# Kernel tuning notes

Measured on AMD Instinct MI355X. Metric: run time of the kernel, lower is better.

Reference implementation:

```python
import jax, jax.numpy as jnp
import numpy as np

B, S, D = 4, 2048, 512
H, HD, RL = 8, 64, 64   # nheads, head_dim = D//H, rl_dim
TEMPER = 1.0
BETA = 1.0
SLOPE = 0.01  # LeakyReLU negative slope
LN_EPS = 1e-5


def setup_inputs() -> dict:
    key = jax.random.key(0)
    ks = jax.random.split(key, 12)
    scale = 0.02
    return {
        "h":   jax.random.normal(ks[0], (B, S, D), dtype=jnp.float32),
        "rh":  jax.random.normal(ks[1], (B, S, RL), dtype=jnp.float32),
        "Wl":  jax.random.normal(ks[2], (D, D), dtype=jnp.float32) * scale,   # linear_l (in,out)
        "Wr":  jax.random.normal(ks[3], (D, D), dtype=jnp.float32) * scale,   # linear_r
        "al":  jax.random.normal(ks[4], (HD,), dtype=jnp.float32) * scale,    # att_l: Linear(head_dim,1)
        "ar":  jax.random.normal(ks[5], (HD,), dtype=jnp.float32) * scale,    # att_r
        "Wrs": jax.random.normal(ks[6], (RL, RL * H), dtype=jnp.float32) * scale,  # r_source
        "Wrt": jax.random.normal(ks[7], (RL, RL * H), dtype=jnp.float32) * scale,  # r_target
        "Wf":  jax.random.normal(ks[8], (D, D), dtype=jnp.float32) * scale,   # linear_final
        "ln_g": jnp.ones((D,), dtype=jnp.float32),
        "ln_b": jnp.zeros((D,), dtype=jnp.float32),
    }


def _layer_norm(x, g, b):
    mu = jnp.mean(x, axis=-1, keepdims=True)
    var = jnp.mean(jnp.square(x - mu), axis=-1, keepdims=True)
    return (x - mu) * jax.lax.rsqrt(var + LN_EPS) * g + b


def reference(h, rh, Wl, Wr, al, ar, Wrs, Wrt, Wf, ln_g, ln_b):
    leaky = lambda x: jnp.where(x >= 0, x, SLOPE * x)
    # projections -> [B, H, S, HD]
    fl = (h @ Wl).reshape(B, S, H, HD).transpose(0, 2, 1, 3)
    fr = (h @ Wr).reshape(B, S, H, HD).transpose(0, 2, 1, 3)
    # additive attention logits: [B,H,S,1] + [B,H,1,S]
    sl = jnp.einsum('bhsd,d->bhs', leaky(fl), al)
    sr = jnp.einsum('bhsd,d->bhs', leaky(fr), ar)
    score = sl[:, :, :, None] + sr[:, :, None, :]
    # relation-embedding bilinear bias: r_k @ r_q -> [B,H,S,S]
    r_k = (rh @ Wrs).reshape(B, S, H, RL).transpose(0, 2, 1, 3)   # [B,H,S,RL]
    r_q = (rh @ Wrt).reshape(B, S, H, RL).transpose(0, 2, 3, 1)   # [B,H,RL,S]
    score = score + BETA * jnp.einsum('bhsr,bhrt->bhst', r_k, r_q)
    score = jax.nn.softmax(score / TEMPER, axis=-1)
    # context and output projection (dropout = 0 -> identity)
    context = jnp.einsum('bhst,bhtd->bhsd', score, fr)
    h_sa = context.transpose(0, 2, 1, 3).reshape(B, S, H * HD)
    fh = h_sa @ Wf
    return _layer_norm(h + fh, ln_g, ln_b)
```

## Files before the change

kernel.cpp:

```cpp
#include <hip/hip_runtime.h>
#include <math.h>

#define B_ 4
#define S_ 2048
#define D_ 512
#define H_ 8
#define HD_ 64
#define RL_ 64
#define LN_EPS 1e-5f
#define SLOPE 0.01f
#define LOG2E 1.4426950408889634f

typedef __attribute__((ext_vector_type(8))) __bf16 bf16x8;
typedef __attribute__((ext_vector_type(4))) float f32x4;

__device__ __forceinline__ float leaky(float x) { return x >= 0.f ? x : SLOPE * x; }

__device__ __forceinline__ ushort f2bf(float f) {
    union { float f; unsigned u; } v; v.f = f;
    unsigned r = v.u + 0x7fffu + ((v.u >> 16) & 1u);
    return (ushort)(r >> 16);
}

__device__ __forceinline__ void g2lds16(const void* g, void* l) {
    __builtin_amdgcn_global_load_lds(
        (const __attribute__((address_space(1))) void*)(uintptr_t)g,
        (__attribute__((address_space(3))) void*)(uintptr_t)l, 16, 0, 0);
}

__global__ __launch_bounds__(256) void prep(
    const float* __restrict__ h, const float* __restrict__ rh,
    const float* __restrict__ Wr, const float* __restrict__ Wf,
    const float* __restrict__ Wrs, const float* __restrict__ Wrt,
    ushort* __restrict__ hb, ushort* __restrict__ rhb,
    ushort* __restrict__ WrT, ushort* __restrict__ WfT,
    ushort* __restrict__ WrsT, ushort* __restrict__ WrtT)
{
    const int bx = blockIdx.x, tid = threadIdx.x;
    if (bx < 4608) {
        const float* in = (bx < 4096) ? h : rh;
        ushort* o = (bx < 4096) ? hb : rhb;
        const int i = (bx < 4096 ? bx : bx - 4096) * 256 + tid;
        const float4 v = ((const float4*)in)[i];
        ushort4 u; u.x = f2bf(v.x); u.y = f2bf(v.y); u.z = f2bf(v.z); u.w = f2bf(v.w);
        ((ushort4*)o)[i] = u;
    } else if (bx < 6656) {
        const float* in = (bx < 5632) ? Wr : Wf;
        ushort* o = (bx < 5632) ? WrT : WfT;
        const int idx = (bx - (bx < 5632 ? 4608 : 5632)) * 256 + tid;
        const int k = idx & 511, n = idx >> 9;
        o[idx] = f2bf(in[k * 512 + n]);
    } else {
        const float* in = (bx < 6784) ? Wrs : Wrt;
        ushort* o = (bx < 6784) ? WrsT : WrtT;
        const int idx = (bx - (bx < 6784 ? 6656 : 6784)) * 256 + tid;
        const int k = idx & 63, n = idx >> 6;
        o[idx] = f2bf(in[k * 512 + n]);
    }
}

template <int MODE>
__global__ __launch_bounds__(256) void mfma_gemm(
    const ushort* __restrict__ A, const ushort* __restrict__ WT,
    void* __restrict__ Cout, float* __restrict__ sred,
    const float* __restrict__ avec, int K, float scale,
    const ushort* __restrict__ WT2, void* __restrict__ Cout2, float scale2)
{
    __shared__ ushort As[64 * 32];
    __shared__ ushort Bs[128 * 32];

    const int tid = threadIdx.x;
    const int lane = tid & 63, w = tid >> 6;
    const int ln = lane & 15, quad = lane >> 4;
    const int wm = w >> 1, wn = w & 1;
    const int m0 = blockIdx.x * 64, n0 = blockIdx.y * 128;

    const ushort* wt = WT; void* co = Cout; float scl = scale;
    if constexpr (MODE == 3) {
        if (blockIdx.z) { wt = WT2; co = Cout2; scl = scale2; }
    }

    const int srA = tid >> 2;
    const int lchA = ((lane & 3) - (srA >> 1)) & 3;
    const ushort* Ag = A + (size_t)(m0 + srA) * K + lchA * 8;
    ushort* AsL = As + (size_t)tid * 8;
    const int srB = w * 32 + (lane >> 2);
    const int lchB = ((lane & 3) - (srB >> 1)) & 3;
    const ushort* Bg0 = wt + (size_t)(n0 + srB) * K + lchB * 8;
    const ushort* Bg1 = Bg0 + (size_t)16 * K;
    ushort* BsL = Bs + srB * 32 + (lane & 3) * 8;

    const int pc = (quad + (ln >> 1)) & 3;

    f32x4 acc[2][4] = {};
    for (int k0 = 0; k0 < K; k0 += 32) {
        __syncthreads();
        g2lds16(Ag, AsL);
        g2lds16(Bg0, BsL); g2lds16(Bg1, BsL + 512);
        Ag += 32; Bg0 += 32; Bg1 += 32;
        __syncthreads();

        bf16x8 af[2], bfr[4];
        #pragma unroll
        for (int mi = 0; mi < 2; ++mi)
            af[mi] = *(const bf16x8*)&As[(wm * 32 + mi * 16 + ln) * 32 + pc * 8];
        #pragma unroll
        for (int ni = 0; ni < 4; ++ni)
            bfr[ni] = *(const bf16x8*)&Bs[(wn * 64 + ni * 16 + ln) * 32 + pc * 8];
        #pragma unroll
        for (int mi = 0; mi < 2; ++mi)
            #pragma unroll
            for (int ni = 0; ni < 4; ++ni)
                acc[mi][ni] = __builtin_amdgcn_mfma_f32_16x16x32_bf16(
                    af[mi], bfr[ni], acc[mi][ni], 0, 0, 0);
    }

    if constexpr (MODE == 0) {
        float* C = (float*)co;
        #pragma unroll
        for (int mi = 0; mi < 2; ++mi) {
            const int row = m0 + wm * 32 + mi * 16 + quad * 4;
            #pragma unroll
            for (int ni = 0; ni < 4; ++ni) {
                const int col = n0 + wn * 64 + ni * 16 + ln;
                #pragma unroll
                for (int r = 0; r < 4; ++r)
                    C[(size_t)(row + r) * 512 + col] = acc[mi][ni][r];
            }
        }
    }
    if constexpr (MODE == 2 || MODE == 3) {
        const int head = blockIdx.y * 2 + wn;
        const int b = m0 >> 11;
        const size_t bh = (size_t)b * H_ + head;
        if constexpr (MODE == 2) {
            ushort* frT = (ushort*)co;
            #pragma unroll
            for (int mi = 0; mi < 2; ++mi) {
                const int s = (m0 & (S_ - 1)) + wm * 32 + mi * 16 + quad * 4;
                #pragma unroll
                for (int ni = 0; ni < 4; ++ni) {
                    const int d = ni * 16 + ln;
                    ushort4 o;
                    o.x = f2bf(acc[mi][ni][0]); o.y = f2bf(acc[mi][ni][1]);
                    o.z = f2bf(acc[mi][ni][2]); o.w = f2bf(acc[mi][ni][3]);
                    *(ushort4*)(frT + (bh * 64 + d) * S_ + s) = o;
                }
            }
            float a4[4];
            #pragma unroll
            for (int ni = 0; ni < 4; ++ni) a4[ni] = avec[ni * 16 + ln];
            #pragma unroll
            for (int mi = 0; mi < 2; ++mi) {
                const int s = (m0 & (S_ - 1)) + wm * 32 + mi * 16 + quad * 4;
                #pragma unroll
                for (int r = 0; r < 4; ++r) {
                    float v = 0.f;
                    #pragma unroll
                    for (int ni = 0; ni < 4; ++ni)
                        v += leaky(acc[mi][ni][r]) * a4[ni];
                    #pragma unroll
                    for (int off = 8; off; off >>= 1) v += __shfl_xor(v, off, 16);
                    if (ln == 0) sred[bh * S_ + s + r] = v * scl;
                }
            }
        }
        if constexpr (MODE == 3) {
            ushort* O = (ushort*)co;
            #pragma unroll
            for (int mi = 0; mi < 2; ++mi) {
                const int s = (m0 & (S_ - 1)) + wm * 32 + mi * 16 + quad * 4;
                #pragma unroll
                for (int ni = 0; ni < 4; ++ni) {
                    const int d = ni * 16 + ln;
                    #pragma unroll
                    for (int r = 0; r < 4; ++r)
                        O[(bh * S_ + s + r) * 64 + d] = f2bf(acc[mi][ni][r] * scl);
                }
            }
        }
    }
}

__global__ __launch_bounds__(256) void attn_mfma(
    const ushort* __restrict__ frT, const ushort* __restrict__ rk,
    const ushort* __restrict__ rq, const float* __restrict__ sr,
    ushort* __restrict__ hsa)
{
    __shared__ ushort RQ[2][64][64];
    __shared__ ushort FT[2][64][64];
    __shared__ ushort PS[8][16][72];
    __shared__ float SRs[S_];

    const int tid = threadIdx.x;
    const int w = tid >> 6;
    const int lane = tid & 63;
    const int ln = lane & 15;
    const int quad = lane >> 4;
    const int b = blockIdx.z, h = blockIdx.y, q0 = blockIdx.x * 128;
    const size_t bh = (size_t)b * H_ + h;

    for (int i = tid; i < S_; i += 256) SRs[i] = sr[bh * S_ + i];

    const ushort* rkb = rk + ((bh * S_ + q0 + w * 32) << 6);
    bf16x8 a[2][2];
    #pragma unroll
    for (int qs = 0; qs < 2; ++qs) {
        const ushort* p = rkb + (qs * 16 + ln) * 64 + quad * 8;
        a[qs][0] = *(const bf16x8*)p;
        a[qs][1] = *(const bf16x8*)(p + 32);
    }

    const ushort* rqb = rq + (bh * S_ << 6);
    const ushort* ftb = frT + (size_t)bh * 64 * S_;

    const int rl = lane >> 3;
    const int sg = ((lane & 7) - rl) & 7;
    const int row0 = w * 16 + rl;

    #define STAGE(buf, t0)                                                        \
        {                                                                         \
            _Pragma("unroll")                                                     \
            for (int i = 0; i < 2; ++i) {                                         \
                const int tr = row0 + i * 8;                                      \
                g2lds16(rqb + ((size_t)((t0) + tr) << 6) + sg * 8,                \
                        &RQ[buf][tr][(lane & 7) * 8]);                            \
                g2lds16(ftb + (size_t)tr * S_ + (t0) + sg * 8,                    \
                        &FT[buf][tr][(lane & 7) * 8]);                            \
            }                                                                     \
        }

    STAGE(0, 0)
    __syncthreads();

    float lsum[2][4] = {};
    f32x4 ctx[2][4] = {};
    int buf = 0;

    for (int t0 = 0; t0 < S_; t0 += 64) {
        if (t0 + 64 < S_) STAGE(buf ^ 1, t0 + 64)

        f32x4 sc[2][4];
        #pragma unroll
        for (int jb = 0; jb < 4; ++jb) {
            const int tr = 16 * jb + ln;
            const bf16x8 b0 = *(const bf16x8*)&RQ[buf][tr][((quad + tr) & 7) * 8];
            const bf16x8 b1 = *(const bf16x8*)&RQ[buf][tr][((quad + 4 + tr) & 7) * 8];
            #pragma unroll
            for (int qs = 0; qs < 2; ++qs) {
                f32x4 t = {0.f, 0.f, 0.f, 0.f};
                t = __builtin_amdgcn_mfma_f32_16x16x32_bf16(a[qs][0], b0, t, 0, 0, 0);
                t = __builtin_amdgcn_mfma_f32_16x16x32_bf16(a[qs][1], b1, t, 0, 0, 0);
                sc[qs][jb] = t;
            }
        }

        float srv[4];
        #pragma unroll
        for (int jb = 0; jb < 4; ++jb) srv[jb] = SRs[t0 + 16 * jb + ln];

        #pragma unroll
        for (int qs = 0; qs < 2; ++qs)
            #pragma unroll
            for (int r = 0; r < 4; ++r) {
                const int prow = quad * 4 + r;
                float psum = 0.f;
                #pragma unroll
                for (int jb = 0; jb < 4; ++jb) {
                    const float p = __builtin_amdgcn_exp2f(sc[qs][jb][r] + srv[jb]);
                    psum += p;
                    union { float f; unsigned u; } v; v.f = p;
                    PS[w * 2 + qs][prow][16 * jb + ln] = (ushort)(v.u >> 16);
                }
                lsum[qs][r] += psum;
            }

        bf16x8 fb0[4], fb1[4];
        #pragma unroll
        for (int jb = 0; jb < 4; ++jb) {
            const int dr = 16 * jb + ln;
            fb0[jb] = *(const bf16x8*)&FT[buf][dr][((quad + dr) & 7) * 8];
            fb1[jb] = *(const bf16x8*)&FT[buf][dr][((quad + 4 + dr) & 7) * 8];
        }
        #pragma unroll
        for (int qs = 0; qs < 2; ++qs) {
            const bf16x8 pa0 = *(const bf16x8*)&PS[w * 2 + qs][ln][quad * 8];
            const bf16x8 pa1 = *(const bf16x8*)&PS[w * 2 + qs][ln][32 + quad * 8];
            #pragma unroll
            for (int jb = 0; jb < 4; ++jb) {
                ctx[qs][jb] = __builtin_amdgcn_mfma_f32_16x16x32_bf16(pa0, fb0[jb], ctx[qs][jb], 0, 0, 0);
                ctx[qs][jb] = __builtin_amdgcn_mfma_f32_16x16x32_bf16(pa1, fb1[jb], ctx[qs][jb], 0, 0, 0);
            }
        }

        __syncthreads();
        buf ^= 1;
    }

    #pragma unroll
    for (int qs = 0; qs < 2; ++qs)
        #pragma unroll
        for (int r = 0; r < 4; ++r) {
            float l = lsum[qs][r];
            #pragma unroll
            for (int off = 8; off; off >>= 1) l += __shfl_xor(l, off, 16);
            const float inv = 1.f / l;
            const int q = q0 + w * 32 + qs * 16 + quad * 4 + r;
            ushort* orow = hsa + (size_t)(b * S_ + q) * D_ + h * 64;
            #pragma unroll
            for (int jb = 0; jb < 4; ++jb)
                orow[16 * jb + ln] = f2bf(ctx[qs][jb][r] * inv);
        }
}

__global__ __launch_bounds__(256) void ln_kernel(
    const float* __restrict__ h, const float* __restrict__ fh,
    const float* __restrict__ g, const float* __restrict__ bb,
    float* __restrict__ out)
{
    const int row = blockIdx.x, tid = threadIdx.x;
    const float* hp = h + (size_t)row * 512;
    const float* fp = fh + (size_t)row * 512;
    const float x0 = hp[tid] + fp[tid];
    const float x1 = hp[tid + 256] + fp[tid + 256];
    __shared__ float red[4];

    float s = x0 + x1;
    #pragma unroll
    for (int off = 32; off; off >>= 1) s += __shfl_xor(s, off, 64);
    if ((tid & 63) == 0) red[tid >> 6] = s;
    __syncthreads();
    const float mu = (red[0] + red[1] + red[2] + red[3]) * (1.f / 512.f);

    const float d0 = x0 - mu, d1 = x1 - mu;
    float v = d0 * d0 + d1 * d1;
    #pragma unroll
    for (int off = 32; off; off >>= 1) v += __shfl_xor(v, off, 64);
    __syncthreads();
    if ((tid & 63) == 0) red[tid >> 6] = v;
    __syncthreads();
    const float var = (red[0] + red[1] + red[2] + red[3]) * (1.f / 512.f);
    const float inv = rsqrtf(var + LN_EPS);

    out[(size_t)row * 512 + tid] = d0 * inv * g[tid] + bb[tid];
    out[(size_t)row * 512 + tid + 256] = d1 * inv * g[tid + 256] + bb[tid + 256];
}

extern "C" void kernel_launch(void* const* d_in, const int* in_sizes, int n_in,
                              void* d_out, int out_size, void* d_ws, size_t ws_size,
                              hipStream_t stream)
{
    const float* h   = (const float*)d_in[0];
    const float* rh  = (const float*)d_in[1];
    const float* Wr  = (const float*)d_in[3];
    const float* ar  = (const float*)d_in[5];
    const float* Wrs = (const float*)d_in[6];
    const float* Wrt = (const float*)d_in[7];
    const float* Wf  = (const float*)d_in[8];
    const float* lng = (const float*)d_in[9];
    const float* lnb = (const float*)d_in[10];
    float* out = (float*)d_out;
    char* wsb  = (char*)d_ws;

    const size_t MB = (size_t)1 << 20;
    ushort* hb   = (ushort*)(wsb);
    ushort* rhb  = (ushort*)(wsb + 8 * MB);
    ushort* WrT  = (ushort*)(wsb + 9 * MB);
    ushort* WfT  = (ushort*)(wsb + 9 * MB + 512 * 1024);
    ushort* WrsT = (ushort*)(wsb + 10 * MB);
    ushort* WrtT = (ushort*)(wsb + 10 * MB + 64 * 1024);
    ushort* frT  = (ushort*)(wsb + 11 * MB);
    ushort* rkw  = (ushort*)(wsb + 19 * MB);
    ushort* rqw  = (ushort*)(wsb + 27 * MB);
    float*  sr   = (float*) (wsb + 35 * MB);
    ushort* hsab = (ushort*)(wsb + 36 * MB);
    float*  fh   = (float*) (wsb + 44 * MB);

    dim3 blk(256);
    prep<<<dim3(6912), blk, 0, stream>>>(h, rh, Wr, Wf, Wrs, Wrt,
                                         hb, rhb, WrT, WfT, WrsT, WrtT);

    dim3 gG(128, 4);
    mfma_gemm<2><<<gG, blk, 0, stream>>>(hb, WrT, frT, sr, ar, 512, LOG2E,
                                         nullptr, nullptr, 0.f);
    mfma_gemm<3><<<dim3(128, 4, 2), blk, 0, stream>>>(
        rhb, WrsT, rkw, nullptr, nullptr, 64, LOG2E, WrtT, rqw, 1.0f);
    attn_mfma<<<dim3(S_ / 128, H_, B_), blk, 0, stream>>>(frT, rkw, rqw, sr, hsab);
    mfma_gemm<0><<<gG, blk, 0, stream>>>(hsab, WfT, fh, nullptr, nullptr, 512, 1.0f,
                                         nullptr, nullptr, 0.f);
    ln_kernel<<<dim3(B_ * S_), blk, 0, stream>>>(h, fh, lng, lnb, out);
}
```

Before: 191.1 us.

## Split prep, tile weight transpose, double-buffer GEMM, shrink attention query tile

```diff
diff --git a/kernel.cpp b/kernel.cpp
--- a/kernel.cpp
+++ b/kernel.cpp
@@ -21,6 +21,9 @@
     unsigned r = v.u + 0x7fffu + ((v.u >> 16) & 1u);
     return (ushort)(r >> 16);
 }
+__device__ __forceinline__ unsigned fbits(float f) {
+    union { float f; unsigned u; } v; v.f = f; return v.u;
+}
 
 __device__ __forceinline__ void g2lds16(const void* g, void* l) {
     __builtin_amdgcn_global_load_lds(
@@ -28,34 +31,49 @@
         (__attribute__((address_space(3))) void*)(uintptr_t)l, 16, 0, 0);
 }
 
-__global__ __launch_bounds__(256) void prep(
+__global__ __launch_bounds__(256) void prep_cast(
     const float* __restrict__ h, const float* __restrict__ rh,
+    ushort* __restrict__ hb, ushort* __restrict__ rhb)
+{
+    const int bx = blockIdx.x, tid = threadIdx.x;
+    const float* in = (bx < 4096) ? h : rh;
+    ushort* o = (bx < 4096) ? hb : rhb;
+    const int i = (bx < 4096 ? bx : bx - 4096) * 256 + tid;
+    const float4 v = ((const float4*)in)[i];
+    ushort4 u; u.x = f2bf(v.x); u.y = f2bf(v.y); u.z = f2bf(v.z); u.w = f2bf(v.w);
+    ((ushort4*)o)[i] = u;
+}
+
+__global__ __launch_bounds__(256) void prep_tr(
     const float* __restrict__ Wr, const float* __restrict__ Wf,
     const float* __restrict__ Wrs, const float* __restrict__ Wrt,
-    ushort* __restrict__ hb, ushort* __restrict__ rhb,
     ushort* __restrict__ WrT, ushort* __restrict__ WfT,
     ushort* __restrict__ WrsT, ushort* __restrict__ WrtT)
 {
-    const int bx = blockIdx.x, tid = threadIdx.x;
-    if (bx < 4608) {
-        const float* in = (bx < 4096) ? h : rh;
-        ushort* o = (bx < 4096) ? hb : rhb;
-        const int i = (bx < 4096 ? bx : bx - 4096) * 256 + tid;
-        const float4 v = ((const float4*)in)[i];
-        ushort4 u; u.x = f2bf(v.x); u.y = f2bf(v.y); u.z = f2bf(v.z); u.w = f2bf(v.w);
-        ((ushort4*)o)[i] = u;
-    } else if (bx < 6656) {
-        const float* in = (bx < 5632) ? Wr : Wf;
-        ushort* o = (bx < 5632) ? WrT : WfT;
-        const int idx = (bx - (bx < 5632 ? 4608 : 5632)) * 256 + tid;
-        const int k = idx & 511, n = idx >> 9;
-        o[idx] = f2bf(in[k * 512 + n]);
-    } else {
-        const float* in = (bx < 6784) ? Wrs : Wrt;
-        ushort* o = (bx < 6784) ? WrsT : WrtT;
-        const int idx = (bx - (bx < 6784 ? 6656 : 6784)) * 256 + tid;
-        const int k = idx & 63, n = idx >> 6;
-        o[idx] = f2bf(in[k * 512 + n]);
+    __shared__ float TS[64][65];
+    int bx = blockIdx.x;
+    const float* in; ushort* out; int K, tk, tn;
+    if (bx < 64)       { in = Wr;  out = WrT;  K = 512; tk = bx & 7; tn = bx >> 3; }
+    else if (bx < 128) { in = Wf;  out = WfT;  K = 512; bx -= 64; tk = bx & 7; tn = bx >> 3; }
+    else if (bx < 136) { in = Wrs; out = WrsT; K = 64;  tk = 0; tn = bx - 128; }
+    else               { in = Wrt; out = WrtT; K = 64;  tk = 0; tn = bx - 136; }
+    const int k0 = tk * 64, n0 = tn * 64;
+    const int r = threadIdx.x >> 4, c4 = (threadIdx.x & 15) * 4;
+    #pragma unroll
+    for (int p = 0; p < 4; ++p) {
+        const int row = r + 16 * p;
+        const float4 v = *(const float4*)(in + (size_t)(k0 + row) * 512 + n0 + c4);
+        TS[row][c4] = v.x; TS[row][c4 + 1] = v.y;
+        TS[row][c4 + 2] = v.z; TS[row][c4 + 3] = v.w;
+    }
+    __syncthreads();
+    #pragma unroll
+    for (int p = 0; p < 4; ++p) {
+        const int nn = r + 16 * p;
+        ushort4 o;
+        o.x = f2bf(TS[c4 + 0][nn]); o.y = f2bf(TS[c4 + 1][nn]);
+        o.z = f2bf(TS[c4 + 2][nn]); o.w = f2bf(TS[c4 + 3][nn]);
+        *(ushort4*)(out + (size_t)(n0 + nn) * K + k0 + c4) = o;
     }
 }
 
@@ -66,8 +84,8 @@
     const float* __restrict__ avec, int K, float scale,
     const ushort* __restrict__ WT2, void* __restrict__ Cout2, float scale2)
 {
-    __shared__ ushort As[64 * 32];
-    __shared__ ushort Bs[128 * 32];
+    __shared__ ushort As[2][64 * 32];
+    __shared__ ushort Bs[2][128 * 32];
 
     const int tid = threadIdx.x;
     const int lane = tid & 63, w = tid >> 6;
@@ -82,37 +100,43 @@
 
     const int srA = tid >> 2;
     const int lchA = ((lane & 3) - (srA >> 1)) & 3;
-    const ushort* Ag = A + (size_t)(m0 + srA) * K + lchA * 8;
-    ushort* AsL = As + (size_t)tid * 8;
+    const ushort* AgB = A + (size_t)(m0 + srA) * K + lchA * 8;
     const int srB = w * 32 + (lane >> 2);
     const int lchB = ((lane & 3) - (srB >> 1)) & 3;
-    const ushort* Bg0 = wt + (size_t)(n0 + srB) * K + lchB * 8;
-    const ushort* Bg1 = Bg0 + (size_t)16 * K;
-    ushort* BsL = Bs + srB * 32 + (lane & 3) * 8;
+    const ushort* BgB0 = wt + (size_t)(n0 + srB) * K + lchB * 8;
+    const ushort* BgB1 = BgB0 + (size_t)16 * K;
+    const int aoff = tid * 8;
+    const int boff = srB * 32 + (lane & 3) * 8;
 
     const int pc = (quad + (ln >> 1)) & 3;
 
+    g2lds16(AgB, &As[0][aoff]);
+    g2lds16(BgB0, &Bs[0][boff]);
+    g2lds16(BgB1, &Bs[0][boff + 512]);
+
     f32x4 acc[2][4] = {};
+    int buf = 0;
     for (int k0 = 0; k0 < K; k0 += 32) {
         __syncthreads();
-        g2lds16(Ag, AsL);
-        g2lds16(Bg0, BsL); g2lds16(Bg1, BsL + 512);
-        Ag += 32; Bg0 += 32; Bg1 += 32;
-        __syncthreads();
-
+        if (k0 + 32 < K) {
+            g2lds16(AgB + k0 + 32, &As[buf ^ 1][aoff]);
+            g2lds16(BgB0 + k0 + 32, &Bs[buf ^ 1][boff]);
+            g2lds16(BgB1 + k0 + 32, &Bs[buf ^ 1][boff + 512]);
+        }
         bf16x8 af[2], bfr[4];
         #pragma unroll
         for (int mi = 0; mi < 2; ++mi)
-            af[mi] = *(const bf16x8*)&As[(wm * 32 + mi * 16 + ln) * 32 + pc * 8];
+            af[mi] = *(const bf16x8*)&As[buf][(wm * 32 + mi * 16 + ln) * 32 + pc * 8];
         #pragma unroll
         for (int ni = 0; ni < 4; ++ni)
-            bfr[ni] = *(const bf16x8*)&Bs[(wn * 64 + ni * 16 + ln) * 32 + pc * 8];
+            bfr[ni] = *(const bf16x8*)&Bs[buf][(wn * 64 + ni * 16 + ln) * 32 + pc * 8];
         #pragma unroll
         for (int mi = 0; mi < 2; ++mi)
             #pragma unroll
             for (int ni = 0; ni < 4; ++ni)
                 acc[mi][ni] = __builtin_amdgcn_mfma_f32_16x16x32_bf16(
                     af[mi], bfr[ni], acc[mi][ni], 0, 0, 0);
+        buf ^= 1;
     }
 
     if constexpr (MODE == 0) {
@@ -182,115 +206,95 @@
     }
 }
 
-__global__ __launch_bounds__(256) void attn_mfma(
+__global__ __launch_bounds__(256, 4) void attn_mfma(
     const ushort* __restrict__ frT, const ushort* __restrict__ rk,
     const ushort* __restrict__ rq, const float* __restrict__ sr,
     ushort* __restrict__ hsa)
 {
     __shared__ ushort RQ[2][64][64];
     __shared__ ushort FT[2][64][64];
-    __shared__ ushort PS[8][16][72];
-    __shared__ float SRs[S_];
+    __shared__ ushort PS[4][16][64];
 
     const int tid = threadIdx.x;
     const int w = tid >> 6;
     const int lane = tid & 63;
     const int ln = lane & 15;
     const int quad = lane >> 4;
-    const int b = blockIdx.z, h = blockIdx.y, q0 = blockIdx.x * 128;
+    const int b = blockIdx.z, h = blockIdx.y, q0 = blockIdx.x * 64;
     const size_t bh = (size_t)b * H_ + h;
 
-    for (int i = tid; i < S_; i += 256) SRs[i] = sr[bh * S_ + i];
-
-    const ushort* rkb = rk + ((bh * S_ + q0 + w * 32) << 6);
-    bf16x8 a[2][2];
-    #pragma unroll
-    for (int qs = 0; qs < 2; ++qs) {
-        const ushort* p = rkb + (qs * 16 + ln) * 64 + quad * 8;
-        a[qs][0] = *(const bf16x8*)p;
-        a[qs][1] = *(const bf16x8*)(p + 32);
-    }
+    const ushort* rkb = rk + ((bh * S_ + q0 + w * 16 + ln) << 6);
+    const bf16x8 a0 = *(const bf16x8*)(rkb + quad * 8);
+    const bf16x8 a1 = *(const bf16x8*)(rkb + 32 + quad * 8);
 
     const ushort* rqb = rq + (bh * S_ << 6);
     const ushort* ftb = frT + (size_t)bh * 64 * S_;
+    const float* srp = sr + bh * S_;
 
     const int rl = lane >> 3;
-    const int sg = ((lane & 7) - rl) & 7;
-    const int row0 = w * 16 + rl;
-
-    #define STAGE(buf, t0)                                                        \
-        {                                                                         \
-            _Pragma("unroll")                                                     \
-            for (int i = 0; i < 2; ++i) {                                         \
-                const int tr = row0 + i * 8;                                      \
-                g2lds16(rqb + ((size_t)((t0) + tr) << 6) + sg * 8,                \
-                        &RQ[buf][tr][(lane & 7) * 8]);                            \
-                g2lds16(ftb + (size_t)tr * S_ + (t0) + sg * 8,                    \
-                        &FT[buf][tr][(lane & 7) * 8]);                            \
-            }                                                                     \
+    const int pg = lane & 7;
+    const int row_b = w * 16 + rl;
+    const int sgF = (pg - rl) & 7;
+    const int sgR0 = (pg - 4 * w - (rl >> 2)) & 7;
+    const int sgR1 = (pg - 4 * w - 2 - (rl >> 2)) & 7;
+
+    #define STAGE(bf, t0)                                                     \
+        {                                                                     \
+            g2lds16(rqb + ((size_t)((t0) + row_b) << 6) + sgR0 * 8,           \
+                    &RQ[bf][row_b][pg * 8]);                                  \
+            g2lds16(rqb + ((size_t)((t0) + row_b + 8) << 6) + sgR1 * 8,       \
+                    &RQ[bf][row_b + 8][pg * 8]);                              \
+            g2lds16(ftb + (size_t)row_b * S_ + (t0) + sgF * 8,                \
+                    &FT[bf][row_b][pg * 8]);                                  \
+            g2lds16(ftb + (size_t)(row_b + 8) * S_ + (t0) + sgF * 8,          \
+                    &FT[bf][row_b + 8][pg * 8]);                              \
         }
 
     STAGE(0, 0)
     __syncthreads();
 
-    float lsum[2][4] = {};
-    f32x4 ctx[2][4] = {};
+    float lsum[4] = {};
+    f32x4 ctx[4] = {};
     int buf = 0;
 
     for (int t0 = 0; t0 < S_; t0 += 64) {
         if (t0 + 64 < S_) STAGE(buf ^ 1, t0 + 64)
-
-        f32x4 sc[2][4];
+        const float4 srv = *(const float4*)(srp + t0 + 4 * ln);
+
+        f32x4 sc[4];
         #pragma unroll
         for (int jb = 0; jb < 4; ++jb) {
-            const int tr = 16 * jb + ln;
-            const bf16x8 b0 = *(const bf16x8*)&RQ[buf][tr][((quad + tr) & 7) * 8];
-            const bf16x8 b1 = *(const bf16x8*)&RQ[buf][tr][((quad + 4 + tr) & 7) * 8];
-            #pragma unroll
-            for (int qs = 0; qs < 2; ++qs) {
-                f32x4 t = {0.f, 0.f, 0.f, 0.f};
-                t = __builtin_amdgcn_mfma_f32_16x16x32_bf16(a[qs][0], b0, t, 0, 0, 0);
-                t = __builtin_amdgcn_mfma_f32_16x16x32_bf16(a[qs][1], b1, t, 0, 0, 0);
-                sc[qs][jb] = t;
-            }
-        }
-
-        float srv[4];
-        #pragma unroll
-        for (int jb = 0; jb < 4; ++jb) srv[jb] = SRs[t0 + 16 * jb + ln];
-
-        #pragma unroll
-        for (int qs = 0; qs < 2; ++qs)
-            #pragma unroll
-            for (int r = 0; r < 4; ++r) {
-                const int prow = quad * 4 + r;
-                float psum = 0.f;
-                #pragma unroll
-                for (int jb = 0; jb < 4; ++jb) {
-                    const float p = __builtin_amdgcn_exp2f(sc[qs][jb][r] + srv[jb]);
-                    psum += p;
-                    union { float f; unsigned u; } v; v.f = p;
-                    PS[w * 2 + qs][prow][16 * jb + ln] = (ushort)(v.u >> 16);
-                }
-                lsum[qs][r] += psum;
-            }
-
-        bf16x8 fb0[4], fb1[4];
+            const int tr = 4 * ln + jb;
+            const bf16x8 b0 = *(const bf16x8*)&RQ[buf][tr][((quad + ln) & 7) * 8];
+            const bf16x8 b1 = *(const bf16x8*)&RQ[buf][tr][((quad + 4 + ln) & 7) * 8];
+            f32x4 t = {0.f, 0.f, 0.f, 0.f};
+            t = __builtin_amdgcn_mfma_f32_16x16x32_bf16(a0, b0, t, 0, 0, 0);
+            t = __builtin_amdgcn_mfma_f32_16x16x32_bf16(a1, b1, t, 0, 0, 0);
+            sc[jb] = t;
+        }
+
+        #pragma unroll
+        for (int r = 0; r < 4; ++r) {
+            const float p0 = __builtin_amdgcn_exp2f(sc[0][r] + srv.x);
+            const float p1 = __builtin_amdgcn_exp2f(sc[1][r] + srv.y);
+            const float p2 = __builtin_amdgcn_exp2f(sc[2][r] + srv.z);
+            const float p3 = __builtin_amdgcn_exp2f(sc[3][r] + srv.w);
+            lsum[r] += (p0 + p1) + (p2 + p3);
+            const unsigned lo = (fbits(p0) >> 16) | (fbits(p1) & 0xffff0000u);
+            const unsigned hi = (fbits(p2) >> 16) | (fbits(p3) & 0xffff0000u);
+            const int prow = quad * 4 + r;
+            *(uint2*)&PS[w][prow][(((ln >> 1) + prow) & 7) * 8 + (ln & 1) * 4] =
+                make_uint2(lo, hi);
+        }
+
+        const bf16x8 pa0 = *(const bf16x8*)&PS[w][ln][((quad + ln) & 7) * 8];
+        const bf16x8 pa1 = *(const bf16x8*)&PS[w][ln][((quad + 4 + ln) & 7) * 8];
         #pragma unroll
         for (int jb = 0; jb < 4; ++jb) {
-            const int dr = 16 * jb + ln;
-            fb0[jb] = *(const bf16x8*)&FT[buf][dr][((quad + dr) & 7) * 8];
-            fb1[jb] = *(const bf16x8*)&FT[buf][dr][((quad + 4 + dr) & 7) * 8];
-        }
-        #pragma unroll
-        for (int qs = 0; qs < 2; ++qs) {
-            const bf16x8 pa0 = *(const bf16x8*)&PS[w * 2 + qs][ln][quad * 8];
-            const bf16x8 pa1 = *(const bf16x8*)&PS[w * 2 + qs][ln][32 + quad * 8];
-            #pragma unroll
-            for (int jb = 0; jb < 4; ++jb) {
-                ctx[qs][jb] = __builtin_amdgcn_mfma_f32_16x16x32_bf16(pa0, fb0[jb], ctx[qs][jb], 0, 0, 0);
-                ctx[qs][jb] = __builtin_amdgcn_mfma_f32_16x16x32_bf16(pa1, fb1[jb], ctx[qs][jb], 0, 0, 0);
-            }
+            const bf16x8 fb0 = *(const bf16x8*)&FT[buf][16 * jb + ln][((quad + ln) & 7) * 8];
+            const bf16x8 fb1 = *(const bf16x8*)&FT[buf][16 * jb + ln][((quad + 4 + ln) & 7) * 8];
+            ctx[jb] = __builtin_amdgcn_mfma_f32_16x16x32_bf16(pa0, fb0, ctx[jb], 0, 0, 0);
+            ctx[jb] = __builtin_amdgcn_mfma_f32_16x16x32_bf16(pa1, fb1, ctx[jb], 0, 0, 0);
         }
 
         __syncthreads();
@@ -298,19 +302,17 @@
     }
 
     #pragma unroll
-    for (int qs = 0; qs < 2; ++qs)
-        #pragma unroll
-        for (int r = 0; r < 4; ++r) {
-            float l = lsum[qs][r];
-            #pragma unroll
-            for (int off = 8; off; off >>= 1) l += __shfl_xor(l, off, 16);
-            const float inv = 1.f / l;
-            const int q = q0 + w * 32 + qs * 16 + quad * 4 + r;
-            ushort* orow = hsa + (size_t)(b * S_ + q) * D_ + h * 64;
-            #pragma unroll
-            for (int jb = 0; jb < 4; ++jb)
-                orow[16 * jb + ln] = f2bf(ctx[qs][jb][r] * inv);
-        }
+    for (int r = 0; r < 4; ++r) {
+        float l = lsum[r];
+        #pragma unroll
+        for (int off = 8; off; off >>= 1) l += __shfl_xor(l, off, 16);
+        const float inv = 1.f / l;
+        const int q = q0 + w * 16 + quad * 4 + r;
+        ushort* orow = hsa + (size_t)(b * S_ + q) * D_ + h * 64;
+        #pragma unroll
+        for (int jb = 0; jb < 4; ++jb)
+            orow[16 * jb + ln] = f2bf(ctx[jb][r] * inv);
+    }
 }
 
 __global__ __launch_bounds__(256) void ln_kernel(
@@ -377,15 +379,15 @@
     float*  fh   = (float*) (wsb + 44 * MB);
 
     dim3 blk(256);
-    prep<<<dim3(6912), blk, 0, stream>>>(h, rh, Wr, Wf, Wrs, Wrt,
-                                         hb, rhb, WrT, WfT, WrsT, WrtT);
+    prep_cast<<<dim3(4608), blk, 0, stream>>>(h, rh, hb, rhb);
+    prep_tr<<<dim3(144), blk, 0, stream>>>(Wr, Wf, Wrs, Wrt, WrT, WfT, WrsT, WrtT);
 
     dim3 gG(128, 4);
     mfma_gemm<2><<<gG, blk, 0, stream>>>(hb, WrT, frT, sr, ar, 512, LOG2E,
                                          nullptr, nullptr, 0.f);
     mfma_gemm<3><<<dim3(128, 4, 2), blk, 0, stream>>>(
         rhb, WrsT, rkw, nullptr, nullptr, 64, LOG2E, WrtT, rqw, 1.0f);
-    attn_mfma<<<dim3(S_ / 128, H_, B_), blk, 0, stream>>>(frT, rkw, rqw, sr, hsab);
+    attn_mfma<<<dim3(S_ / 64, H_, B_), blk, 0, stream>>>(frT, rkw, rqw, sr, hsab);
     mfma_gemm<0><<<gG, blk, 0, stream>>>(hsab, WfT, fh, nullptr, nullptr, 512, 1.0f,
                                          nullptr, nullptr, 0.f);
     ln_kernel<<<dim3(B_ * S_), blk, 0, stream>>>(h, fh, lng, lnb, out);
```

New measurement: 184.6 us. -3.4%, faster.
